# Performance work log

Hardware: AMD Instinct MI355X
Metric: run time of the kernel (lower is better)

The kernel has to match this reference:

```python
import jax, jax.numpy as jnp
import numpy as np

B, S, D, H = 2, 2048, 1024, 16
HD = D // H
NEG = -1000000.0


def setup_inputs() -> dict:
    key = jax.random.key(0)
    ks = jax.random.split(key, 8)
    sc = 1.0 / np.sqrt(D)
    return {
        "q": jax.random.normal(ks[0], (B, S, D), dtype=jnp.float32),
        "k": jax.random.normal(ks[1], (B, S, D), dtype=jnp.float32),
        "v": jax.random.normal(ks[2], (B, S, D), dtype=jnp.float32),
        "valid_lens": jax.random.randint(ks[3], (B,), 1, S + 1, dtype=jnp.int32),
        "Wq": jax.random.normal(ks[4], (D, D), dtype=jnp.float32) * sc,
        "Wk": jax.random.normal(ks[5], (D, D), dtype=jnp.float32) * sc,
        "Wv": jax.random.normal(ks[6], (D, D), dtype=jnp.float32) * sc,
        "Wo": jax.random.normal(ks[7], (D, D), dtype=jnp.float32) * sc,
    }


def reference(q, k, v, valid_lens, Wq, Wk, Wv, Wo):
    # projections: [B,S,D] -> [B,H,S,HD]
    def split_heads(x):
        return x.reshape(B, S, H, HD).transpose(0, 2, 1, 3)

    qh = split_heads(q @ Wq)
    kh = split_heads(k @ Wk)
    vh = split_heads(v @ Wv)

    # scaled dot-product scores: [B,H,Sq,Sk]
    scores = jnp.einsum("bhqd,bhkd->bhqk", qh, kh) / jnp.sqrt(
        jnp.asarray(HD, dtype=jnp.float32))

    # sequence mask over key axis: positions >= valid_len replaced by -1e6
    key_pos = jnp.arange(S, dtype=jnp.int32)
    mask = key_pos[None, :] < valid_lens[:, None]            # [B,Sk]
    scores = jnp.where(mask[:, None, None, :], scores, NEG)

    attn = jax.nn.softmax(scores, axis=-1)                   # dropout rate 0
    ctx = jnp.einsum("bhqk,bhkd->bhqd", attn, vh)            # [B,H,S,HD]
    out = ctx.transpose(0, 2, 1, 3).reshape(B, S, D)
    return out @ Wo
```

## Files before the change

kernel.cpp:

```cpp
#include <hip/hip_runtime.h>
#include <math.h>

#define NB 2
#define NS 2048
#define ND 1024
#define NH 16
#define NHD 64
#define GK 1024
#define NEG -1000000.0f

typedef __attribute__((ext_vector_type(4))) float f32x4;
typedef __attribute__((ext_vector_type(8))) _Float16 f16x8;
typedef __attribute__((ext_vector_type(4))) _Float16 f16x4;

typedef const __attribute__((address_space(1))) unsigned int* gas_t;
typedef __attribute__((address_space(3))) unsigned int* las_t;

__global__ __launch_bounds__(256) void wt_kernel(const float* __restrict__ Wq,
                                                 const float* __restrict__ Wk,
                                                 const float* __restrict__ Wv,
                                                 const float* __restrict__ Wo,
                                                 _Float16* __restrict__ WtBase) {
  __shared__ _Float16 Ts[64][72];
  const int which = blockIdx.x >> 8;
  const int rem = blockIdx.x & 255;
  const int tk = rem >> 4;
  const int tn = rem & 15;
  const float* W = which == 0 ? Wq : which == 1 ? Wk : which == 2 ? Wv : Wo;
  _Float16* Wt = WtBase + (size_t)which * (GK * ND);
  const int t = threadIdx.x;
#pragma unroll
  for (int p = 0; p < 4; ++p) {
    const int kr = (p << 4) + (t >> 4);
    const int nc = (t & 15) << 2;
    float4 v = *(const float4*)(W + (size_t)((tk << 6) + kr) * ND + (tn << 6) + nc);
    f16x4 h = {(_Float16)v.x, (_Float16)v.y, (_Float16)v.z, (_Float16)v.w};
    *(f16x4*)&Ts[kr][nc] = h;
  }
  __syncthreads();
#pragma unroll
  for (int p = 0; p < 4; ++p) {
    const int nr = (p << 4) + (t >> 4);
    const int kc = (t & 15) << 2;
    f16x4 h;
#pragma unroll
    for (int u = 0; u < 4; ++u) h[u] = Ts[kc + u][nr];
    *(f16x4*)(Wt + (size_t)((tn << 6) + nr) * GK + (tk << 6) + kc) = h;
  }
}

__global__ __launch_bounds__(256) void proj_kernel(const float* __restrict__ xq,
                                                   const float* __restrict__ xk,
                                                   const float* __restrict__ xv,
                                                   const _Float16* __restrict__ WtBase,
                                                   _Float16* __restrict__ Qh,
                                                   _Float16* __restrict__ Kh,
                                                   _Float16* __restrict__ VhT) {
  constexpr int BK = 32;
  __shared__ alignas(16) _Float16 As[128 * BK];
  __shared__ alignas(16) _Float16 Bs[128 * BK];

  int idx = ((blockIdx.x % 96) << 3) + (blockIdx.x / 96);
  const int which = idx >> 8;
  idx &= 255;
  const int bm = (idx >> 3) << 7;
  const int bn = (idx & 7) << 7;
  const float* A = which == 0 ? xq : which == 1 ? xk : xv;
  const _Float16* Bt = WtBase + (size_t)which * (ND * GK);

  const int tid = threadIdx.x, lane = tid & 63, w = tid >> 6;
  const int i16 = lane & 15, g4 = lane >> 4;
  const int wr = w >> 1, wc = w & 1;

  f32x4 acc[4][4] = {};

  for (int kt = 0; kt < GK / BK; ++kt) {
#pragma unroll
    for (int u = 0; u < 2; ++u) {
      const int c = (((w << 1) + u) << 6) + lane;
      const int r = c >> 2, sl = c & 3;
      const float* src = A + (size_t)(bm + r) * GK + (kt << 5) + ((sl ^ (r & 3)) << 3);
      float4 v0 = *(const float4*)src;
      float4 v1 = *(const float4*)(src + 4);
      f16x8 h;
#pragma unroll
      for (int j = 0; j < 4; ++j) { h[j] = (_Float16)v0[j]; h[4 + j] = (_Float16)v1[j]; }
      *(f16x8*)&As[(r << 5) + (sl << 3)] = h;
    }
#pragma unroll
    for (int u = 0; u < 2; ++u) {
      const int cb = ((w << 1) + u) << 6;
      const int c = cb + lane;
      const int r = c >> 2, sl = c & 3;
      __builtin_amdgcn_global_load_lds(
          (gas_t)(const void*)(Bt + (size_t)(bn + r) * GK + (kt << 5) + ((sl ^ (r & 3)) << 3)),
          (las_t)(void*)&Bs[cb << 3], 16, 0, 0);
    }
    __syncthreads();

    f16x8 af[4], bf[4];
#pragma unroll
    for (int mi = 0; mi < 4; ++mi) {
      const int r = (wr << 6) + (mi << 4) + i16;
      af[mi] = *(const f16x8*)&As[(r << 5) + ((g4 ^ (r & 3)) << 3)];
    }
#pragma unroll
    for (int ni = 0; ni < 4; ++ni) {
      const int r = (wc << 6) + (ni << 4) + i16;
      bf[ni] = *(const f16x8*)&Bs[(r << 5) + ((g4 ^ (r & 3)) << 3)];
    }
#pragma unroll
    for (int mi = 0; mi < 4; ++mi)
#pragma unroll
      for (int ni = 0; ni < 4; ++ni)
        acc[mi][ni] = __builtin_amdgcn_mfma_f32_16x16x32_f16(af[mi], bf[ni], acc[mi][ni], 0, 0, 0);
    __syncthreads();
  }

  if (which == 2) {
#pragma unroll
    for (int mi = 0; mi < 4; ++mi)
#pragma unroll
      for (int ni = 0; ni < 4; ++ni) {
        const int row0 = bm + (wr << 6) + (mi << 4) + (g4 << 2);
        const int col = bn + (wc << 6) + (ni << 4) + i16;
        const int bb = row0 >> 11, ss = row0 & (NS - 1);
        const int hh = col >> 6, dd = col & 63;
        f16x4 hv;
#pragma unroll
        for (int j = 0; j < 4; ++j) hv[j] = (_Float16)acc[mi][ni][j];
        *(f16x4*)&VhT[(((size_t)(bb * NH + hh) * NHD + dd) << 11) + ss] = hv;
      }
  } else {
    const float scale = which == 0 ? 0.125f : 1.0f;
    _Float16* Out = which == 0 ? Qh : Kh;
#pragma unroll
    for (int mi = 0; mi < 4; ++mi)
#pragma unroll
      for (int ni = 0; ni < 4; ++ni)
#pragma unroll
        for (int j = 0; j < 4; ++j) {
          const int row = bm + (wr << 6) + (mi << 4) + (g4 << 2) + j;
          const int col = bn + (wc << 6) + (ni << 4) + i16;
          const int bb = row >> 11, ss = row & (NS - 1);
          const int hh = col >> 6, dd = col & 63;
          Out[(((size_t)(bb * NH + hh) * NS + ss) << 6) + dd] = (_Float16)(acc[mi][ni][j] * scale);
        }
  }
}

__global__ __launch_bounds__(256) void attn_kernel(_Float16* __restrict__ Qc,
                                                   const _Float16* __restrict__ Kh,
                                                   const _Float16* __restrict__ VhT,
                                                   const int* __restrict__ valid_lens) {
  __shared__ alignas(16) _Float16 Ks[2][4096];
  __shared__ alignas(16) _Float16 Vt[2][4096];
  __shared__ alignas(16) _Float16 Ps[64][72];

  const int b0 = blockIdx.x;
  const int idx = ((b0 & 7) << 5) + ((b0 >> 8) << 8) + ((b0 >> 3) & 31);
  const int bh = idx >> 5, qt = idx & 31;
  const int valid = valid_lens[bh >> 4];
  const int tid = threadIdx.x, lane = tid & 63, w = tid >> 6;
  const int i16 = lane & 15, g4 = lane >> 4;

  _Float16* Qb = Qc + ((size_t)bh * NS + (qt << 6)) * NHD;
  const _Float16* Kb = Kh + (size_t)bh * NS * NHD;
  const _Float16* Vb = VhT + (size_t)bh * NHD * NS;

  f16x8 qf[2];
#pragma unroll
  for (int dc = 0; dc < 2; ++dc)
    qf[dc] = *(const f16x8*)(Qb + (size_t)((w << 4) + i16) * NHD + (dc << 5) + (g4 << 3));

  f32x4 acc[4] = {};
  float mrow[4] = {-1e30f, -1e30f, -1e30f, -1e30f};
  float lsum[4] = {0.f, 0.f, 0.f, 0.f};

  auto STAGE = [&](int buf, int t) {
#pragma unroll
    for (int u = 0; u < 2; ++u) {
      const int cb = ((w << 1) + u) << 6;
      const int c = cb + lane;
      const int r = c >> 3, sl = c & 7;
      const int so = (sl ^ (r & 7)) << 3;
      __builtin_amdgcn_global_load_lds(
          (gas_t)(const void*)(Kb + (size_t)((t << 6) + r) * NHD + so),
          (las_t)(void*)&Ks[buf][cb << 3], 16, 0, 0);
      __builtin_amdgcn_global_load_lds(
          (gas_t)(const void*)(Vb + (size_t)r * NS + (t << 6) + so),
          (las_t)(void*)&Vt[buf][cb << 3], 16, 0, 0);
    }
  };

  const int ntiles = (valid + 63) >> 6;
  STAGE(0, 0);

  for (int t = 0; t < ntiles; ++t) {
    __syncthreads();
    if (t + 1 < ntiles) STAGE((t + 1) & 1, t + 1);
    const int buf = t & 1;
    const bool full = ((t + 1) << 6) <= valid;

    float pj[4][4];
#pragma unroll
    for (int cf = 0; cf < 4; ++cf) {
      f32x4 sa = {};
      const int r = (cf << 4) + i16;
#pragma unroll
      for (int dc = 0; dc < 2; ++dc) {
        f16x8 kf = *(const f16x8*)&Ks[buf][(r << 6) + ((((dc << 2) + g4) ^ (r & 7)) << 3)];
        sa = __builtin_amdgcn_mfma_f32_16x16x32_f16(qf[dc], kf, sa, 0, 0, 0);
      }
      if (full) {
#pragma unroll
        for (int j = 0; j < 4; ++j) pj[cf][j] = sa[j];
      } else {
        const int kvcol = (t << 6) + r;
#pragma unroll
        for (int j = 0; j < 4; ++j) pj[cf][j] = (kvcol >= valid) ? NEG : sa[j];
      }
    }

    float tmax[4];
#pragma unroll
    for (int j = 0; j < 4; ++j)
      tmax[j] = fmaxf(fmaxf(pj[0][j], pj[1][j]), fmaxf(pj[2][j], pj[3][j]));
    for (int off = 1; off < 16; off <<= 1)
#pragma unroll
      for (int j = 0; j < 4; ++j)
        tmax[j] = fmaxf(tmax[j], __shfl_xor(tmax[j], off, 64));

    float rowsum[4] = {0.f, 0.f, 0.f, 0.f};
#pragma unroll
    for (int j = 0; j < 4; ++j) {
      const float mn = fmaxf(mrow[j], tmax[j]);
      const float scv = __expf(mrow[j] - mn);
      mrow[j] = mn;
      lsum[j] *= scv;
#pragma unroll
      for (int dn = 0; dn < 4; ++dn) acc[dn][j] *= scv;
    }
#pragma unroll
    for (int cf = 0; cf < 4; ++cf)
#pragma unroll
      for (int j = 0; j < 4; ++j) {
        const float p = __expf(pj[cf][j] - mrow[j]);
        rowsum[j] += p;
        Ps[(w << 4) + (g4 << 2) + j][(cf << 4) + i16] = (_Float16)p;
      }
    for (int off = 1; off < 16; off <<= 1)
#pragma unroll
      for (int j = 0; j < 4; ++j)
        rowsum[j] += __shfl_xor(rowsum[j], off, 64);
#pragma unroll
    for (int j = 0; j < 4; ++j) lsum[j] += rowsum[j];

#pragma unroll
    for (int ks = 0; ks < 2; ++ks) {
      f16x8 pf = *(const f16x8*)&Ps[(w << 4) + i16][(ks << 5) + (g4 << 3)];
#pragma unroll
      for (int dn = 0; dn < 4; ++dn) {
        const int d = (dn << 4) + i16;
        f16x8 vf = *(const f16x8*)&Vt[buf][(d << 6) + ((((ks << 2) + g4) ^ (d & 7)) << 3)];
        acc[dn] = __builtin_amdgcn_mfma_f32_16x16x32_f16(pf, vf, acc[dn], 0, 0, 0);
      }
    }
  }

#pragma unroll
  for (int dn = 0; dn < 4; ++dn)
#pragma unroll
    for (int j = 0; j < 4; ++j) {
      const int qrow = (w << 4) + (g4 << 2) + j;
      Qb[(size_t)qrow * NHD + (dn << 4) + i16] = (_Float16)(acc[dn][j] / lsum[j]);
    }
}

__global__ __launch_bounds__(256) void out_kernel(const _Float16* __restrict__ ctx,
                                                  const _Float16* __restrict__ Wot,
                                                  float* __restrict__ Out) {
  constexpr int BK = 32;
  __shared__ alignas(16) _Float16 As[128 * BK];
  __shared__ alignas(16) _Float16 Bs[64 * BK];

  const int idx = ((blockIdx.x % 64) << 3) + (blockIdx.x / 64);
  const int bm = (idx >> 4) << 7;
  const int bn = (idx & 15) << 6;

  const int tid = threadIdx.x, lane = tid & 63, w = tid >> 6;
  const int i16 = lane & 15, g4 = lane >> 4;
  const int wr = w >> 1, wc = w & 1;

  f32x4 acc[4][2] = {};

  for (int kt = 0; kt < GK / BK; ++kt) {
#pragma unroll
    for (int u = 0; u < 2; ++u) {
      const int cb = ((w << 1) + u) << 6;
      const int c = cb + lane;
      const int r = c >> 2, sl = c & 3;
      const int m = bm + r;
      const int kcol = (kt << 5) + ((sl ^ (r & 3)) << 3);
      const int bb = m >> 11, ss = m & (NS - 1);
      const int hh = kcol >> 6, dd = kcol & 63;
      __builtin_amdgcn_global_load_lds(
          (gas_t)(const void*)(ctx + (((size_t)(bb * NH + hh) * NS + ss) << 6) + dd),
          (las_t)(void*)&As[cb << 3], 16, 0, 0);
    }
    {
      const int cb = w << 6;
      const int c = cb + lane;
      const int r = c >> 2, sl = c & 3;
      __builtin_amdgcn_global_load_lds(
          (gas_t)(const void*)(Wot + (size_t)(bn + r) * GK + (kt << 5) + ((sl ^ (r & 3)) << 3)),
          (las_t)(void*)&Bs[cb << 3], 16, 0, 0);
    }
    __syncthreads();

    f16x8 af[4], bf[2];
#pragma unroll
    for (int mi = 0; mi < 4; ++mi) {
      const int r = (wr << 6) + (mi << 4) + i16;
      af[mi] = *(const f16x8*)&As[(r << 5) + ((g4 ^ (r & 3)) << 3)];
    }
#pragma unroll
    for (int ni = 0; ni < 2; ++ni) {
      const int r = (wc << 5) + (ni << 4) + i16;
      bf[ni] = *(const f16x8*)&Bs[(r << 5) + ((g4 ^ (r & 3)) << 3)];
    }
#pragma unroll
    for (int mi = 0; mi < 4; ++mi)
#pragma unroll
      for (int ni = 0; ni < 2; ++ni)
        acc[mi][ni] = __builtin_amdgcn_mfma_f32_16x16x32_f16(af[mi], bf[ni], acc[mi][ni], 0, 0, 0);
    __syncthreads();
  }

#pragma unroll
  for (int mi = 0; mi < 4; ++mi)
#pragma unroll
    for (int ni = 0; ni < 2; ++ni)
#pragma unroll
      for (int j = 0; j < 4; ++j) {
        const int row = bm + (wr << 6) + (mi << 4) + (g4 << 2) + j;
        const int col = bn + (wc << 5) + (ni << 4) + i16;
        Out[(size_t)row * ND + col] = acc[mi][ni][j];
      }
}

extern "C" void kernel_launch(void* const* d_in, const int* in_sizes, int n_in,
                              void* d_out, int out_size, void* d_ws, size_t ws_size,
                              hipStream_t stream) {
  const float* q  = (const float*)d_in[0];
  const float* k  = (const float*)d_in[1];
  const float* v  = (const float*)d_in[2];
  const int*   vl = (const int*)d_in[3];
  const float* Wq = (const float*)d_in[4];
  const float* Wk = (const float*)d_in[5];
  const float* Wv = (const float*)d_in[6];
  const float* Wo = (const float*)d_in[7];

  _Float16* ws = (_Float16*)d_ws;
  _Float16* Qh  = ws;
  _Float16* Kh  = ws + 4194304;
  _Float16* VhT = ws + 8388608;
  _Float16* Wt  = ws + 12582912;

  wt_kernel<<<dim3(1024), dim3(256), 0, stream>>>(Wq, Wk, Wv, Wo, Wt);
  proj_kernel<<<dim3(768), dim3(256), 0, stream>>>(q, k, v, Wt, Qh, Kh, VhT);
  attn_kernel<<<dim3(NB * NH * (NS >> 6)), dim3(256), 0, stream>>>(Qh, Kh, VhT, vl);
  out_kernel<<<dim3(512), dim3(256), 0, stream>>>(Qh, Wt + 3145728, (float*)d_out);
}
```

Before: 226.1 us.

## Transpose QK^T MFMA, use exp2 softmax with lazy rescale and packed P stores

The attention kernel swaps the MFMA operands so each lane holds one query row's scores. Row max and sum then need only two cross-lane shuffles instead of a 16-lane butterfly. Softmax uses exp2 with log2(e) folded into the Q projection scale, and the running-max rescale is skipped unless some row's max grows by more than 8. P is packed to fp16 with cvt_pkrtz into a swizzled LDS buffer, and the proj kernel's block-index swizzle is reordered. The lazy rescale can leave unnormalised values up to 2^8 in fp16 P, and the final normalisation becomes a reciprocal multiply.

```diff
diff --git a/kernel.cpp b/kernel.cpp
--- a/kernel.cpp
+++ b/kernel.cpp
@@ -12,15 +12,16 @@
 typedef __attribute__((ext_vector_type(4))) float f32x4;
 typedef __attribute__((ext_vector_type(8))) _Float16 f16x8;
 typedef __attribute__((ext_vector_type(4))) _Float16 f16x4;
+typedef __attribute__((ext_vector_type(2))) __fp16 fp16x2_t;
 
 typedef const __attribute__((address_space(1))) unsigned int* gas_t;
 typedef __attribute__((address_space(3))) unsigned int* las_t;
 
-__global__ __launch_bounds__(256) void wt_kernel(const float* __restrict__ Wq,
-                                                 const float* __restrict__ Wk,
-                                                 const float* __restrict__ Wv,
-                                                 const float* __restrict__ Wo,
-                                                 _Float16* __restrict__ WtBase) {
+__global__ __launch_bounds__(256) void prep_kernel(const float* __restrict__ Wq,
+                                                   const float* __restrict__ Wk,
+                                                   const float* __restrict__ Wv,
+                                                   const float* __restrict__ Wo,
+                                                   _Float16* __restrict__ WtBase) {
   __shared__ _Float16 Ts[64][72];
   const int which = blockIdx.x >> 8;
   const int rem = blockIdx.x & 255;
@@ -56,15 +57,15 @@
                                                    _Float16* __restrict__ Qh,
                                                    _Float16* __restrict__ Kh,
                                                    _Float16* __restrict__ VhT) {
-  constexpr int BK = 32;
-  __shared__ alignas(16) _Float16 As[128 * BK];
-  __shared__ alignas(16) _Float16 Bs[128 * BK];
-
-  int idx = ((blockIdx.x % 96) << 3) + (blockIdx.x / 96);
-  const int which = idx >> 8;
-  idx &= 255;
-  const int bm = (idx >> 3) << 7;
-  const int bn = (idx & 7) << 7;
+  __shared__ alignas(16) _Float16 As[128 * 32];
+  __shared__ alignas(16) _Float16 Bs[128 * 32];
+
+  const int b = blockIdx.x;
+  const int wg = ((b & 7) * 96) + (b >> 3);
+  const int which = wg >> 8;
+  const int rem = wg & 255;
+  const int bm = (rem >> 3) << 7;
+  const int bn = (rem & 7) << 7;
   const float* A = which == 0 ? xq : which == 1 ? xk : xv;
   const _Float16* Bt = WtBase + (size_t)which * (ND * GK);
 
@@ -74,7 +75,7 @@
 
   f32x4 acc[4][4] = {};
 
-  for (int kt = 0; kt < GK / BK; ++kt) {
+  for (int kt = 0; kt < GK / 32; ++kt) {
 #pragma unroll
     for (int u = 0; u < 2; ++u) {
       const int c = (((w << 1) + u) << 6) + lane;
@@ -84,7 +85,7 @@
       float4 v1 = *(const float4*)(src + 4);
       f16x8 h;
 #pragma unroll
-      for (int j = 0; j < 4; ++j) { h[j] = (_Float16)v0[j]; h[4 + j] = (_Float16)v1[j]; }
+      for (int j = 0; j < 4; ++j) { h[j] = (_Float16)(&v0.x)[j]; h[4 + j] = (_Float16)(&v1.x)[j]; }
       *(f16x8*)&As[(r << 5) + (sl << 3)] = h;
     }
 #pragma unroll
@@ -132,8 +133,8 @@
         *(f16x4*)&VhT[(((size_t)(bb * NH + hh) * NHD + dd) << 11) + ss] = hv;
       }
   } else {
-    const float scale = which == 0 ? 0.125f : 1.0f;
-    _Float16* Out = which == 0 ? Qh : Kh;
+    const float scale = (which == 0) ? 0.125f * 1.44269504f : 1.0f;
+    _Float16* Out = (which == 0) ? Qh : Kh;
 #pragma unroll
     for (int mi = 0; mi < 4; ++mi)
 #pragma unroll
@@ -155,7 +156,7 @@
                                                    const int* __restrict__ valid_lens) {
   __shared__ alignas(16) _Float16 Ks[2][4096];
   __shared__ alignas(16) _Float16 Vt[2][4096];
-  __shared__ alignas(16) _Float16 Ps[64][72];
+  __shared__ alignas(16) unsigned int PsW[2048];
 
   const int b0 = blockIdx.x;
   const int idx = ((b0 & 7) << 5) + ((b0 >> 8) << 8) + ((b0 >> 3) & 31);
@@ -163,6 +164,7 @@
   const int valid = valid_lens[bh >> 4];
   const int tid = threadIdx.x, lane = tid & 63, w = tid >> 6;
   const int i16 = lane & 15, g4 = lane >> 4;
+  const int qrow = (w << 4) + i16;
 
   _Float16* Qb = Qc + ((size_t)bh * NS + (qt << 6)) * NHD;
   const _Float16* Kb = Kh + (size_t)bh * NS * NHD;
@@ -171,11 +173,11 @@
   f16x8 qf[2];
 #pragma unroll
   for (int dc = 0; dc < 2; ++dc)
-    qf[dc] = *(const f16x8*)(Qb + (size_t)((w << 4) + i16) * NHD + (dc << 5) + (g4 << 3));
+    qf[dc] = *(const f16x8*)(Qb + (size_t)qrow * NHD + (dc << 5) + (g4 << 3));
 
   f32x4 acc[4] = {};
-  float mrow[4] = {-1e30f, -1e30f, -1e30f, -1e30f};
-  float lsum[4] = {0.f, 0.f, 0.f, 0.f};
+  float mrow = -1e30f;
+  float lsum = 0.f;
 
   auto STAGE = [&](int buf, int t) {
 #pragma unroll
@@ -210,55 +212,63 @@
 #pragma unroll
       for (int dc = 0; dc < 2; ++dc) {
         f16x8 kf = *(const f16x8*)&Ks[buf][(r << 6) + ((((dc << 2) + g4) ^ (r & 7)) << 3)];
-        sa = __builtin_amdgcn_mfma_f32_16x16x32_f16(qf[dc], kf, sa, 0, 0, 0);
+        sa = __builtin_amdgcn_mfma_f32_16x16x32_f16(kf, qf[dc], sa, 0, 0, 0);
       }
       if (full) {
 #pragma unroll
         for (int j = 0; j < 4; ++j) pj[cf][j] = sa[j];
       } else {
-        const int kvcol = (t << 6) + r;
-#pragma unroll
-        for (int j = 0; j < 4; ++j) pj[cf][j] = (kvcol >= valid) ? NEG : sa[j];
-      }
-    }
-
-    float tmax[4];
-#pragma unroll
-    for (int j = 0; j < 4; ++j)
-      tmax[j] = fmaxf(fmaxf(pj[0][j], pj[1][j]), fmaxf(pj[2][j], pj[3][j]));
-    for (int off = 1; off < 16; off <<= 1)
-#pragma unroll
-      for (int j = 0; j < 4; ++j)
-        tmax[j] = fmaxf(tmax[j], __shfl_xor(tmax[j], off, 64));
-
-    float rowsum[4] = {0.f, 0.f, 0.f, 0.f};
-#pragma unroll
-    for (int j = 0; j < 4; ++j) {
-      const float mn = fmaxf(mrow[j], tmax[j]);
-      const float scv = __expf(mrow[j] - mn);
-      mrow[j] = mn;
-      lsum[j] *= scv;
-#pragma unroll
-      for (int dn = 0; dn < 4; ++dn) acc[dn][j] *= scv;
-    }
+        const int kvb = (t << 6) + (cf << 4) + (g4 << 2);
+#pragma unroll
+        for (int j = 0; j < 4; ++j) pj[cf][j] = (kvb + j >= valid) ? NEG : sa[j];
+      }
+    }
+
+    float m16 = pj[0][0];
 #pragma unroll
     for (int cf = 0; cf < 4; ++cf)
 #pragma unroll
+      for (int j = 0; j < 4; ++j) m16 = fmaxf(m16, pj[cf][j]);
+    m16 = fmaxf(m16, __shfl_xor(m16, 16, 64));
+    m16 = fmaxf(m16, __shfl_xor(m16, 32, 64));
+
+    if (__any(m16 > mrow + 8.0f)) {
+      const float mn = fmaxf(mrow, m16);
+      const float scv = __builtin_amdgcn_exp2f(mrow - mn);
+      mrow = mn;
+      lsum *= scv;
+#pragma unroll
       for (int j = 0; j < 4; ++j) {
-        const float p = __expf(pj[cf][j] - mrow[j]);
-        rowsum[j] += p;
-        Ps[(w << 4) + (g4 << 2) + j][(cf << 4) + i16] = (_Float16)p;
-      }
-    for (int off = 1; off < 16; off <<= 1)
-#pragma unroll
-      for (int j = 0; j < 4; ++j)
-        rowsum[j] += __shfl_xor(rowsum[j], off, 64);
-#pragma unroll
-    for (int j = 0; j < 4; ++j) lsum[j] += rowsum[j];
+        const float sj = __shfl(scv, (g4 << 2) + j, 64);
+#pragma unroll
+        for (int dn = 0; dn < 4; ++dn) acc[dn][j] *= sj;
+      }
+    }
+
+    float rsum = 0.f;
+#pragma unroll
+    for (int cf = 0; cf < 4; ++cf) {
+      float p0 = __builtin_amdgcn_exp2f(pj[cf][0] - mrow);
+      float p1 = __builtin_amdgcn_exp2f(pj[cf][1] - mrow);
+      float p2 = __builtin_amdgcn_exp2f(pj[cf][2] - mrow);
+      float p3 = __builtin_amdgcn_exp2f(pj[cf][3] - mrow);
+      rsum += (p0 + p1) + (p2 + p3);
+      union { fp16x2_t h; unsigned int u; } ca, cb2;
+      ca.h = __builtin_amdgcn_cvt_pkrtz(p0, p1);
+      cb2.h = __builtin_amdgcn_cvt_pkrtz(p2, p3);
+      const int u8 = (cf << 2) + g4;
+      const int s16 = (u8 >> 1) ^ (qrow & 7);
+      uint2 dv; dv.x = ca.u; dv.y = cb2.u;
+      *(uint2*)&PsW[(qrow << 5) + (s16 << 2) + ((u8 & 1) << 1)] = dv;
+    }
+    rsum += __shfl_xor(rsum, 16, 64);
+    rsum += __shfl_xor(rsum, 32, 64);
+    lsum += rsum;
 
 #pragma unroll
     for (int ks = 0; ks < 2; ++ks) {
-      f16x8 pf = *(const f16x8*)&Ps[(w << 4) + i16][(ks << 5) + (g4 << 3)];
+      const int cr = (ks << 2) + g4;
+      f16x8 pf = *(const f16x8*)&PsW[(qrow << 5) + ((cr ^ (qrow & 7)) << 2)];
 #pragma unroll
       for (int dn = 0; dn < 4; ++dn) {
         const int d = (dn << 4) + i16;
@@ -268,12 +278,16 @@
     }
   }
 
+  float linv[4];
+#pragma unroll
+  for (int j = 0; j < 4; ++j)
+    linv[j] = 1.0f / __shfl(lsum, (g4 << 2) + j, 64);
 #pragma unroll
   for (int dn = 0; dn < 4; ++dn)
 #pragma unroll
     for (int j = 0; j < 4; ++j) {
-      const int qrow = (w << 4) + (g4 << 2) + j;
-      Qb[(size_t)qrow * NHD + (dn << 4) + i16] = (_Float16)(acc[dn][j] / lsum[j]);
+      const int qr = (w << 4) + (g4 << 2) + j;
+      Qb[(size_t)qr * NHD + (dn << 4) + i16] = (_Float16)(acc[dn][j] * linv[j]);
     }
 }
 
@@ -367,7 +381,7 @@
   _Float16* VhT = ws + 8388608;
   _Float16* Wt  = ws + 12582912;
 
-  wt_kernel<<<dim3(1024), dim3(256), 0, stream>>>(Wq, Wk, Wv, Wo, Wt);
+  prep_kernel<<<dim3(1024), dim3(256), 0, stream>>>(Wq, Wk, Wv, Wo, Wt);
   proj_kernel<<<dim3(768), dim3(256), 0, stream>>>(q, k, v, Wt, Qh, Kh, VhT);
   attn_kernel<<<dim3(NB * NH * (NS >> 6)), dim3(256), 0, stream>>>(Qh, Kh, VhT, vl);
   out_kernel<<<dim3(512), dim3(256), 0, stream>>>(Qh, Wt + 3145728, (float*)d_out);
```

New measurement: 203.2 us. -10.1%, faster.
